# Kernel tuning notes

Hardware: AMD Instinct MI355X
Metric: run time of the kernel (lower is better)

Reference implementation:

```python
import jax, jax.numpy as jnp
import numpy as np

N_NODES = 50000
N_EDGES = 600000
D = 128        # input_dim == hidden_dim
OUT = 2        # output_dim
N_LAYERS = 6


def setup_inputs() -> dict:
    key = jax.random.key(0)
    ks = jax.random.split(key, 6)
    scale = 1.0 / np.sqrt(D)
    x = jax.random.normal(ks[0], (N_NODES, D), jnp.float32)
    edge_index = jax.random.randint(ks[1], (2, N_EDGES), 0, N_NODES)
    Wl = jax.random.normal(ks[2], (N_LAYERS, D, D), jnp.float32) * scale  # neighbor (lin_l) weights
    Wr = jax.random.normal(ks[3], (N_LAYERS, D, D), jnp.float32) * scale  # root (lin_r) weights
    bl = jnp.zeros((N_LAYERS, D), jnp.float32)                            # lin_l bias
    fc_W = jax.random.normal(ks[4], (D, OUT), jnp.float32) * scale
    fc_b = jnp.zeros((OUT,), jnp.float32)
    return {"x": x, "edge_index": edge_index, "Wl": Wl, "Wr": Wr, "bl": bl,
            "fc_W": fc_W, "fc_b": fc_b}


def _sage_conv(h, src, dst, deg_inv, Wl_i, Wr_i, bl_i):
    # mean aggregation over incoming edges: gather -> scatter-add -> normalize
    agg = jax.ops.segment_sum(h[src], dst, num_segments=h.shape[0]) * deg_inv  # [N, D]
    return agg @ Wl_i + h @ Wr_i + bl_i


def reference(x, edge_index, Wl, Wr, bl, fc_W, fc_b):
    src, dst = edge_index[0], edge_index[1]
    deg = jax.ops.segment_sum(jnp.ones(src.shape, x.dtype), dst, num_segments=x.shape[0])
    deg_inv = (1.0 / jnp.maximum(deg, 1.0))[:, None]  # [N, 1]
    h = x
    # ReLU follows every SAGEConv: inner act of each GraphSAGE block + explicit F.relu after each block
    for i in range(N_LAYERS):
        h = _sage_conv(h, src, dst, deg_inv, Wl[i], Wr[i], bl[i])
        h = jax.nn.relu(h)
    return h @ fc_W + fc_b  # [N, OUT]
```

## Files before the change

kernel.cpp:

```cpp
#include <hip/hip_runtime.h>
#include <hip/hip_bf16.h>

#define N_NODES 50000
#define N_EDGES 600000
#define DD 128
#define N_LAYERS 6
#define SCAN_BLOCKS 196
#define N_CHUNKS 3125

#define XB16_T 1600000
#define ZERO_T 50000
#define PREPW_T 196608
#define PREP_TOTAL (XB16_T + ZERO_T + PREPW_T)

typedef __attribute__((ext_vector_type(8))) short bf16x8;
typedef __attribute__((ext_vector_type(4))) float floatx4;

__device__ __forceinline__ void ldsdma16(const void* g, void* l) {
    __builtin_amdgcn_global_load_lds(
        (const __attribute__((address_space(1))) char*)g,
        (__attribute__((address_space(3))) char*)l, 16, 0, 0);
}

__device__ __forceinline__ unsigned short f2b(float f) {
    unsigned u = __float_as_uint(f);
    unsigned r = (u + 0x7FFFu + ((u >> 16) & 1u)) >> 16;
    return (unsigned short)r;
}


__global__ void prep_all(const float* __restrict__ x, unsigned short* __restrict__ hx,
                         const float* __restrict__ Wl, const float* __restrict__ Wr,
                         unsigned short* __restrict__ WT2,
                         int* __restrict__ deg, int* __restrict__ cursor) {
    int gid = blockIdx.x * blockDim.x + threadIdx.x;
    if (gid < XB16_T) {
        int b = gid * 4;
        float4 v = *(const float4*)(x + b);
        ushort4 o;
        o.x = f2b(v.x); o.y = f2b(v.y); o.z = f2b(v.z); o.w = f2b(v.w);
        *(ushort4*)(hx + b) = o;
    } else if (gid < XB16_T + ZERO_T) {
        int i = gid - XB16_T;
        deg[i] = 0; cursor[i] = 0;
    } else if (gid < PREP_TOTAL) {
        int idx = gid - (XB16_T + ZERO_T);
        int l   = idx >> 15;
        int rem = idx & 32767;
        int n   = rem >> 8;
        int k2  = rem & 255;
        const float* W = (k2 < 128 ? Wl : Wr) + (size_t)l * DD * DD + (size_t)(k2 & 127) * DD + n;
        WT2[idx] = f2b(*W);
    }
}


__global__ void count_deg(const int* __restrict__ dst, int* __restrict__ deg) {
    int e = blockIdx.x * blockDim.x + threadIdx.x;
    if (e < N_EDGES) atomicAdd(&deg[dst[e]], 1);
}

__global__ void block_sums(const int* __restrict__ deg, int* __restrict__ bsum) {
    __shared__ int s[256];
    int tid = threadIdx.x;
    int i = blockIdx.x * 256 + tid;
    int v = (i < N_NODES) ? deg[i] : 0;
    s[tid] = v;
    __syncthreads();
    #pragma unroll
    for (int off = 128; off > 0; off >>= 1) {
        if (tid < off) s[tid] += s[tid + off];
        __syncthreads();
    }
    if (tid == 0) bsum[blockIdx.x] = s[0];
}

__global__ void scan_bsums(int* __restrict__ bsum, int* __restrict__ offsets) {
    __shared__ int s[256];
    int tid = threadIdx.x;
    int v = (tid < SCAN_BLOCKS) ? bsum[tid] : 0;
    s[tid] = v;
    __syncthreads();
    for (int off = 1; off < 256; off <<= 1) {
        int t = (tid >= off) ? s[tid - off] : 0;
        __syncthreads();
        s[tid] += t;
        __syncthreads();
    }
    if (tid < SCAN_BLOCKS) bsum[tid] = s[tid] - v;
    if (tid == 0) offsets[N_NODES] = N_EDGES;
}

__global__ void write_offsets(const int* __restrict__ deg, const int* __restrict__ bsum,
                              int* __restrict__ offsets, float* __restrict__ deg_inv) {
    __shared__ int s[256];
    int tid = threadIdx.x;
    int i = blockIdx.x * 256 + tid;
    int v = (i < N_NODES) ? deg[i] : 0;
    s[tid] = v;
    __syncthreads();
    for (int off = 1; off < 256; off <<= 1) {
        int t = (tid >= off) ? s[tid - off] : 0;
        __syncthreads();
        s[tid] += t;
        __syncthreads();
    }
    if (i < N_NODES) {
        offsets[i] = bsum[blockIdx.x] + s[tid] - v;
        deg_inv[i] = 1.0f / (float)(v > 1 ? v : 1);
    }
}

__global__ void fill_csr(const int* __restrict__ src, const int* __restrict__ dst,
                         const int* __restrict__ offsets, int* __restrict__ cursor,
                         int* __restrict__ csr_src) {
    int e = blockIdx.x * blockDim.x + threadIdx.x;
    if (e < N_EDGES) {
        int d = dst[e];
        int p = atomicAdd(&cursor[d], 1);
        csr_src[offsets[d] + p] = src[e];
    }
}


__global__ void aggregate(const unsigned short* __restrict__ hin, const int* __restrict__ offsets,
                          const int* __restrict__ csr_src, const float* __restrict__ deg_inv,
                          unsigned short* __restrict__ agg) {
    int wid  = threadIdx.x >> 6;
    int lane = threadIdx.x & 63;
    int grp  = lane >> 4;
    int l16  = lane & 15;
    int b = blockIdx.x;
    int x = b & 7, s = b >> 3;
    int group = 4 * (x + 8 * (s >> 2)) + (s & 3);
    int node = group * 4 + wid;
    if (node >= N_NODES) return;
    int s0 = offsets[node], e0 = offsets[node + 1];

    float a0=0,a1=0,a2=0,a3=0,a4=0,a5=0,a6=0,a7=0;
    for (int j = s0 + grp; j < e0; j += 4) {
        int src = csr_src[j];
        uint4 v = *(const uint4*)(hin + (size_t)src * DD + l16 * 8);
        a0 += __uint_as_float(v.x << 16); a1 += __uint_as_float(v.x & 0xFFFF0000u);
        a2 += __uint_as_float(v.y << 16); a3 += __uint_as_float(v.y & 0xFFFF0000u);
        a4 += __uint_as_float(v.z << 16); a5 += __uint_as_float(v.z & 0xFFFF0000u);
        a6 += __uint_as_float(v.w << 16); a7 += __uint_as_float(v.w & 0xFFFF0000u);
    }
    a0 += __shfl_xor(a0, 16, 64); a1 += __shfl_xor(a1, 16, 64);
    a2 += __shfl_xor(a2, 16, 64); a3 += __shfl_xor(a3, 16, 64);
    a4 += __shfl_xor(a4, 16, 64); a5 += __shfl_xor(a5, 16, 64);
    a6 += __shfl_xor(a6, 16, 64); a7 += __shfl_xor(a7, 16, 64);
    a0 += __shfl_xor(a0, 32, 64); a1 += __shfl_xor(a1, 32, 64);
    a2 += __shfl_xor(a2, 32, 64); a3 += __shfl_xor(a3, 32, 64);
    a4 += __shfl_xor(a4, 32, 64); a5 += __shfl_xor(a5, 32, 64);
    a6 += __shfl_xor(a6, 32, 64); a7 += __shfl_xor(a7, 32, 64);

    if (grp == 0) {
        float di = deg_inv[node];
        uint4 o;
        o.x = (unsigned)f2b(a0 * di) | ((unsigned)f2b(a1 * di) << 16);
        o.y = (unsigned)f2b(a2 * di) | ((unsigned)f2b(a3 * di) << 16);
        o.z = (unsigned)f2b(a4 * di) | ((unsigned)f2b(a5 * di) << 16);
        o.w = (unsigned)f2b(a6 * di) | ((unsigned)f2b(a7 * di) << 16);
        *(uint4*)(agg + (size_t)node * DD + l16 * 8) = o;
    }
}


__launch_bounds__(512, 2)
__global__ void gemm_resW(const unsigned short* __restrict__ Agg,
                          const unsigned short* __restrict__ H,
                          const unsigned short* __restrict__ WT2,
                          const float* __restrict__ bias,
                          unsigned short* __restrict__ Cout,
                          const float* __restrict__ fcW,
                          const float* __restrict__ fcb,
                          float* __restrict__ out,
                          int doFC) {
    __shared__ __align__(16) unsigned short sW[128 * 256];
    __shared__ __align__(16) unsigned short sA[8][4096];

    int tid  = threadIdx.x;
    int wid  = tid >> 6, lane = tid & 63;
    int l15  = lane & 15, q = lane >> 4;

    for (int t = tid; t < 4096; t += 512) {
        int col = t >> 5, c = t & 31;
        uint4 v = *(const uint4*)(WT2 + (size_t)col * 256 + c * 8);
        *(uint4*)(sW + ((size_t)col * 32 + (c ^ (col & 7))) * 8) = v;
    }
    __syncthreads();

    float bcol[8];
    #pragma unroll
    for (int j = 0; j < 8; ++j) bcol[j] = bias[j * 16 + l15];

    float2 fcw[8];
    float fb0 = 0.f, fb1 = 0.f;
    if (doFC) {
        #pragma unroll
        for (int j = 0; j < 8; ++j) fcw[j] = *(const float2*)(fcW + (j * 16 + l15) * 2);
        fb0 = fcb[0]; fb1 = fcb[1];
    }

    unsigned short* myA = &sA[wid][0];
    int x = blockIdx.x & 7, bb = blockIdx.x >> 3;

    for (int chunk = x + 8 * (bb * 8 + wid); chunk < N_CHUNKS; chunk += 2048) {
        int row0 = chunk * 16;
        #pragma unroll
        for (int i = 0; i < 4; ++i) {
            int r  = i * 4 + q;
            int cg = l15 ^ (r & 7);
            ldsdma16(Agg + (size_t)(row0 + r) * DD + cg * 8, myA + (size_t)i * 512 + lane * 8);
        }
        #pragma unroll
        for (int i = 0; i < 4; ++i) {
            int r  = i * 4 + q;
            int cg = l15 ^ (r & 7);
            ldsdma16(H + (size_t)(row0 + r) * DD + cg * 8, myA + 2048 + (size_t)i * 512 + lane * 8);
        }
        __builtin_amdgcn_s_waitcnt(0);

        floatx4 acc[8];
        #pragma unroll
        for (int j = 0; j < 8; ++j) acc[j] = (floatx4){0.f, 0.f, 0.f, 0.f};

        #pragma unroll
        for (int s = 0; s < 8; ++s) {
            int cglob = s * 4 + q;
            int reg   = cglob >> 4;
            int cin   = cglob & 15;
            bf16x8 aF = *(const bf16x8*)(myA + (size_t)reg * 2048 +
                                         ((size_t)l15 * 16 + (cin ^ (l15 & 7))) * 8);
            #pragma unroll
            for (int j = 0; j < 8; ++j) {
                int col = j * 16 + l15;
                bf16x8 bF = *(const bf16x8*)(sW + ((size_t)col * 32 + (cglob ^ (col & 7))) * 8);
                acc[j] = __builtin_amdgcn_mfma_f32_16x16x32_bf16(aF, bF, acc[j], 0, 0, 0);
            }
        }

        if (!doFC) {
            #pragma unroll
            for (int r = 0; r < 4; ++r) {
                int row = row0 + q * 4 + r;
                #pragma unroll
                for (int j = 0; j < 8; ++j) {
                    float v = acc[j][r] + bcol[j];
                    Cout[(size_t)row * DD + j * 16 + l15] = f2b(fmaxf(v, 0.f));
                }
            }
        } else {
            #pragma unroll
            for (int r = 0; r < 4; ++r) {
                float p0 = 0.f, p1 = 0.f;
                #pragma unroll
                for (int j = 0; j < 8; ++j) {
                    float v = fmaxf(acc[j][r] + bcol[j], 0.f);
                    p0 += v * fcw[j].x;
                    p1 += v * fcw[j].y;
                }
                p0 += __shfl_xor(p0, 1, 64); p1 += __shfl_xor(p1, 1, 64);
                p0 += __shfl_xor(p0, 2, 64); p1 += __shfl_xor(p1, 2, 64);
                p0 += __shfl_xor(p0, 4, 64); p1 += __shfl_xor(p1, 4, 64);
                p0 += __shfl_xor(p0, 8, 64); p1 += __shfl_xor(p1, 8, 64);
                if (l15 == 0) {
                    int row = row0 + q * 4 + r;
                    out[row * 2]     = p0 + fb0;
                    out[row * 2 + 1] = p1 + fb1;
                }
            }
        }
    }
}


extern "C" void kernel_launch(void* const* d_in, const int* in_sizes, int n_in,
                              void* d_out, int out_size, void* d_ws, size_t ws_size,
                              hipStream_t stream) {
    const float* x    = (const float*)d_in[0];
    const int*   ei   = (const int*)d_in[1];
    const float* Wl   = (const float*)d_in[2];
    const float* Wr   = (const float*)d_in[3];
    const float* bl   = (const float*)d_in[4];
    const float* fcW  = (const float*)d_in[5];
    const float* fcb  = (const float*)d_in[6];
    float* out = (float*)d_out;

    const int* srcIdx = ei;
    const int* dstIdx = ei + N_EDGES;

    char* ws = (char*)d_ws;
    size_t off = 0;
    auto bump = [&](size_t bytes) { char* p = ws + off; off = (off + bytes + 255) & ~(size_t)255; return p; };
    int*   deg     = (int*)  bump(N_NODES * 4);
    int*   cursor  = (int*)  bump(N_NODES * 4);
    int*   offsets = (int*)  bump((N_NODES + 1) * 4);
    int*   bsum    = (int*)  bump(SCAN_BLOCKS * 4);
    float* deg_inv = (float*)bump(N_NODES * 4);
    int*   csr     = (int*)  bump(N_EDGES * 4);
    unsigned short* hx   = (unsigned short*)bump((size_t)N_NODES * DD * 2);
    unsigned short* hb0  = (unsigned short*)bump((size_t)N_NODES * DD * 2);
    unsigned short* hb1  = (unsigned short*)bump((size_t)N_NODES * DD * 2);
    unsigned short* agg  = (unsigned short*)bump((size_t)N_NODES * DD * 2);
    unsigned short* WT2  = (unsigned short*)bump((size_t)N_LAYERS * 128 * 256 * 2);
    (void)ws_size;

    prep_all<<<(PREP_TOTAL + 255) / 256, 256, 0, stream>>>(x, hx, Wl, Wr, WT2, deg, cursor);
    count_deg<<<(N_EDGES + 255) / 256, 256, 0, stream>>>(dstIdx, deg);
    block_sums<<<SCAN_BLOCKS, 256, 0, stream>>>(deg, bsum);
    scan_bsums<<<1, 256, 0, stream>>>(bsum, offsets);
    write_offsets<<<SCAN_BLOCKS, 256, 0, stream>>>(deg, bsum, offsets, deg_inv);
    fill_csr<<<(N_EDGES + 255) / 256, 256, 0, stream>>>(srcIdx, dstIdx, offsets, cursor, csr);

    const unsigned short* hin = hx;
    unsigned short* hbuf[2] = { hb0, hb1 };
    for (int l = 0; l < N_LAYERS; ++l) {
        int last = (l == N_LAYERS - 1);
        aggregate<<<12512, 256, 0, stream>>>(hin, offsets, csr, deg_inv, agg);
        unsigned short* hout = hbuf[l & 1];
        gemm_resW<<<256, 512, 0, stream>>>(
            agg, hin, WT2 + (size_t)l * 128 * 256, bl + (size_t)l * DD, hout,
            fcW, fcb, out, last);
        hin = hout;
    }
}
```

Baseline: 392.7 us.

## Process two nodes per wavefront in aggregation with 32-byte loads and 2x unroll

The mean-aggregation kernel now maps two nodes to each 64-lane wavefront. Each lane loads 32 bytes of a neighbor row instead of 16, and the edge loop is unrolled by two so more gathers are in flight per lane. Half the blocks are launched and the cross-group reduction shuffles are cut to two steps. In exchange each lane holds 16 accumulators, which raises register pressure, and fewer lanes work per node, which can lengthen the tail for high-degree nodes.

```diff
diff --git a/kernel.cpp b/kernel.cpp
--- a/kernel.cpp
+++ b/kernel.cpp
@@ -7,6 +7,7 @@
 #define N_LAYERS 6
 #define SCAN_BLOCKS 196
 #define N_CHUNKS 3125
+#define AGG_BLOCKS 6256
 
 #define XB16_T 1600000
 #define ZERO_T 50000
@@ -126,43 +127,84 @@
 __global__ void aggregate(const unsigned short* __restrict__ hin, const int* __restrict__ offsets,
                           const int* __restrict__ csr_src, const float* __restrict__ deg_inv,
                           unsigned short* __restrict__ agg) {
-    int wid  = threadIdx.x >> 6;
+    int w    = threadIdx.x >> 6;
     int lane = threadIdx.x & 63;
-    int grp  = lane >> 4;
-    int l16  = lane & 15;
+    int nodeSel = lane >> 5;
+    int l32  = lane & 31;
+    int grp  = l32 >> 3;
+    int p    = l32 & 7;
+
     int b = blockIdx.x;
     int x = b & 7, s = b >> 3;
-    int group = 4 * (x + 8 * (s >> 2)) + (s & 3);
-    int node = group * 4 + wid;
+    int hc = 16 * (s >> 1) + 2 * x + (s & 1);
+    int node = hc * 8 + 2 * w + nodeSel;
     if (node >= N_NODES) return;
     int s0 = offsets[node], e0 = offsets[node + 1];
-
-    float a0=0,a1=0,a2=0,a3=0,a4=0,a5=0,a6=0,a7=0;
-    for (int j = s0 + grp; j < e0; j += 4) {
-        int src = csr_src[j];
-        uint4 v = *(const uint4*)(hin + (size_t)src * DD + l16 * 8);
-        a0 += __uint_as_float(v.x << 16); a1 += __uint_as_float(v.x & 0xFFFF0000u);
-        a2 += __uint_as_float(v.y << 16); a3 += __uint_as_float(v.y & 0xFFFF0000u);
-        a4 += __uint_as_float(v.z << 16); a5 += __uint_as_float(v.z & 0xFFFF0000u);
-        a6 += __uint_as_float(v.w << 16); a7 += __uint_as_float(v.w & 0xFFFF0000u);
-    }
-    a0 += __shfl_xor(a0, 16, 64); a1 += __shfl_xor(a1, 16, 64);
-    a2 += __shfl_xor(a2, 16, 64); a3 += __shfl_xor(a3, 16, 64);
-    a4 += __shfl_xor(a4, 16, 64); a5 += __shfl_xor(a5, 16, 64);
-    a6 += __shfl_xor(a6, 16, 64); a7 += __shfl_xor(a7, 16, 64);
-    a0 += __shfl_xor(a0, 32, 64); a1 += __shfl_xor(a1, 32, 64);
-    a2 += __shfl_xor(a2, 32, 64); a3 += __shfl_xor(a3, 32, 64);
-    a4 += __shfl_xor(a4, 32, 64); a5 += __shfl_xor(a5, 32, 64);
-    a6 += __shfl_xor(a6, 32, 64); a7 += __shfl_xor(a7, 32, 64);
+    float di = deg_inv[node];
+
+    float a[16];
+    #pragma unroll
+    for (int i = 0; i < 16; ++i) a[i] = 0.f;
+
+    const unsigned short* base = hin;
+    int j = s0 + grp;
+    for (; j + 4 < e0; j += 8) {
+        int src1 = csr_src[j];
+        int src2 = csr_src[j + 4];
+        const uint4* r1 = (const uint4*)(base + (size_t)src1 * DD + p * 16);
+        const uint4* r2 = (const uint4*)(base + (size_t)src2 * DD + p * 16);
+        uint4 v1a = r1[0], v1b = r1[1];
+        uint4 v2a = r2[0], v2b = r2[1];
+        a[0] += __uint_as_float(v1a.x << 16); a[1] += __uint_as_float(v1a.x & 0xFFFF0000u);
+        a[2] += __uint_as_float(v1a.y << 16); a[3] += __uint_as_float(v1a.y & 0xFFFF0000u);
+        a[4] += __uint_as_float(v1a.z << 16); a[5] += __uint_as_float(v1a.z & 0xFFFF0000u);
+        a[6] += __uint_as_float(v1a.w << 16); a[7] += __uint_as_float(v1a.w & 0xFFFF0000u);
+        a[8] += __uint_as_float(v1b.x << 16); a[9] += __uint_as_float(v1b.x & 0xFFFF0000u);
+        a[10]+= __uint_as_float(v1b.y << 16); a[11]+= __uint_as_float(v1b.y & 0xFFFF0000u);
+        a[12]+= __uint_as_float(v1b.z << 16); a[13]+= __uint_as_float(v1b.z & 0xFFFF0000u);
+        a[14]+= __uint_as_float(v1b.w << 16); a[15]+= __uint_as_float(v1b.w & 0xFFFF0000u);
+        a[0] += __uint_as_float(v2a.x << 16); a[1] += __uint_as_float(v2a.x & 0xFFFF0000u);
+        a[2] += __uint_as_float(v2a.y << 16); a[3] += __uint_as_float(v2a.y & 0xFFFF0000u);
+        a[4] += __uint_as_float(v2a.z << 16); a[5] += __uint_as_float(v2a.z & 0xFFFF0000u);
+        a[6] += __uint_as_float(v2a.w << 16); a[7] += __uint_as_float(v2a.w & 0xFFFF0000u);
+        a[8] += __uint_as_float(v2b.x << 16); a[9] += __uint_as_float(v2b.x & 0xFFFF0000u);
+        a[10]+= __uint_as_float(v2b.y << 16); a[11]+= __uint_as_float(v2b.y & 0xFFFF0000u);
+        a[12]+= __uint_as_float(v2b.z << 16); a[13]+= __uint_as_float(v2b.z & 0xFFFF0000u);
+        a[14]+= __uint_as_float(v2b.w << 16); a[15]+= __uint_as_float(v2b.w & 0xFFFF0000u);
+    }
+    if (j < e0) {
+        int src1 = csr_src[j];
+        const uint4* r1 = (const uint4*)(base + (size_t)src1 * DD + p * 16);
+        uint4 v1a = r1[0], v1b = r1[1];
+        a[0] += __uint_as_float(v1a.x << 16); a[1] += __uint_as_float(v1a.x & 0xFFFF0000u);
+        a[2] += __uint_as_float(v1a.y << 16); a[3] += __uint_as_float(v1a.y & 0xFFFF0000u);
+        a[4] += __uint_as_float(v1a.z << 16); a[5] += __uint_as_float(v1a.z & 0xFFFF0000u);
+        a[6] += __uint_as_float(v1a.w << 16); a[7] += __uint_as_float(v1a.w & 0xFFFF0000u);
+        a[8] += __uint_as_float(v1b.x << 16); a[9] += __uint_as_float(v1b.x & 0xFFFF0000u);
+        a[10]+= __uint_as_float(v1b.y << 16); a[11]+= __uint_as_float(v1b.y & 0xFFFF0000u);
+        a[12]+= __uint_as_float(v1b.z << 16); a[13]+= __uint_as_float(v1b.z & 0xFFFF0000u);
+        a[14]+= __uint_as_float(v1b.w << 16); a[15]+= __uint_as_float(v1b.w & 0xFFFF0000u);
+    }
+
+    #pragma unroll
+    for (int i = 0; i < 16; ++i) {
+        a[i] += __shfl_xor(a[i], 8, 64);
+        a[i] += __shfl_xor(a[i], 16, 64);
+    }
 
     if (grp == 0) {
-        float di = deg_inv[node];
-        uint4 o;
-        o.x = (unsigned)f2b(a0 * di) | ((unsigned)f2b(a1 * di) << 16);
-        o.y = (unsigned)f2b(a2 * di) | ((unsigned)f2b(a3 * di) << 16);
-        o.z = (unsigned)f2b(a4 * di) | ((unsigned)f2b(a5 * di) << 16);
-        o.w = (unsigned)f2b(a6 * di) | ((unsigned)f2b(a7 * di) << 16);
-        *(uint4*)(agg + (size_t)node * DD + l16 * 8) = o;
+        uint4 o1, o2;
+        o1.x = (unsigned)f2b(a[0] * di) | ((unsigned)f2b(a[1] * di) << 16);
+        o1.y = (unsigned)f2b(a[2] * di) | ((unsigned)f2b(a[3] * di) << 16);
+        o1.z = (unsigned)f2b(a[4] * di) | ((unsigned)f2b(a[5] * di) << 16);
+        o1.w = (unsigned)f2b(a[6] * di) | ((unsigned)f2b(a[7] * di) << 16);
+        o2.x = (unsigned)f2b(a[8] * di) | ((unsigned)f2b(a[9] * di) << 16);
+        o2.y = (unsigned)f2b(a[10]* di) | ((unsigned)f2b(a[11]* di) << 16);
+        o2.z = (unsigned)f2b(a[12]* di) | ((unsigned)f2b(a[13]* di) << 16);
+        o2.w = (unsigned)f2b(a[14]* di) | ((unsigned)f2b(a[15]* di) << 16);
+        uint4* dst = (uint4*)(agg + (size_t)node * DD + p * 16);
+        dst[0] = o1;
+        dst[1] = o2;
     }
 }
 
@@ -318,7 +360,7 @@
     unsigned short* hbuf[2] = { hb0, hb1 };
     for (int l = 0; l < N_LAYERS; ++l) {
         int last = (l == N_LAYERS - 1);
-        aggregate<<<12512, 256, 0, stream>>>(hin, offsets, csr, deg_inv, agg);
+        aggregate<<<AGG_BLOCKS, 256, 0, stream>>>(hin, offsets, csr, deg_inv, agg);
         unsigned short* hout = hbuf[l & 1];
         gemm_resW<<<256, 512, 0, stream>>>(
             agg, hin, WT2 + (size_t)l * 128 * 256, bl + (size_t)l * DD, hout,
```

Result: faster. 347.4 us (-11.6%).
